# Kernel tuning notes

Hardware: AMD Instinct MI355X
Metric: run time of the kernel (lower is better)

The kernel has to match this reference:

```python
import jax, jax.numpy as jnp
import numpy as np
from jax import lax

C, H, W = 16, 1536, 1536
KS = 5    # shift kernel size
PS = 17   # patch size (odd -> conv with padding PS//2 returns exactly HxW)


def setup_inputs() -> dict:
    key = jax.random.key(0)
    ks = jax.random.split(key, 8)
    return {
        "key_vec": jax.random.normal(ks[0], (C,), jnp.float32),
        "beta": jax.random.normal(ks[1], (), jnp.float32),
        "gate": jax.random.normal(ks[2], (), jnp.float32),
        "shift": jax.random.normal(ks[3], (KS, KS), jnp.float32),
        "sharpen": jax.random.normal(ks[4], (), jnp.float32),
        "prev_weights": jax.random.uniform(ks[5], (H, W), jnp.float32),
        "patch": jax.random.normal(ks[6], (C, PS, PS), jnp.float32),
        "mem": jax.random.normal(ks[7], (C, H, W), jnp.float32),
    }


def _address(key_vec, beta, gate, shift, sharpen, prev_weights, mem):
    eps = 1e-8
    c, h, w = mem.shape
    flat_mem = mem.reshape(c, -1).T                       # [HW, C]
    key_norm = key_vec / jnp.maximum(jnp.linalg.norm(key_vec), eps)
    mem_norm = flat_mem / jnp.maximum(
        jnp.linalg.norm(flat_mem, axis=1, keepdims=True), eps)
    content_sim = mem_norm @ key_norm                      # [HW]
    beta_pos = jax.nn.softplus(beta)
    w_c = jax.nn.softmax(beta_pos * content_sim)
    g = jax.nn.sigmoid(gate)
    w_g = g * w_c + (1.0 - g) * prev_weights.reshape(-1)
    # circular-shift convolution (torch conv2d = cross-correlation)
    sk = jax.nn.softmax(shift.reshape(-1)).reshape(shift.shape)
    pad = sk.shape[0] // 2
    padded = jnp.pad(w_g.reshape(h, w), ((pad, pad), (pad, pad)), mode="wrap")
    shifted = lax.conv_general_dilated(
        padded[None, None], sk[None, None], (1, 1), "VALID",
        dimension_numbers=("NCHW", "OIHW", "NCHW"))[0, 0]   # [H, W]
    zeta = jax.nn.softplus(sharpen) + 1.0
    w_pow = jnp.clip(shifted, 1e-8, None) ** zeta
    return w_pow / jnp.maximum(w_pow.sum(), 1e-6)          # [H, W]


def _apply_weighted_patch(weights, patch):
    # torch: conv2d(weights, flipped patch, padding=center) == true convolution,
    # i.e. scatter-add of patch at every cell scaled by weights.
    s = patch.shape[-1]
    center = s // 2
    kernels = patch[:, ::-1, ::-1][:, None]                # [C, 1, S, S]
    out = lax.conv_general_dilated(
        weights[None, None], kernels, (1, 1),
        [(center, center), (center, center)],
        dimension_numbers=("NCHW", "OIHW", "NCHW"))[0]     # [C, H, W]
    return out


def reference(key_vec, beta, gate, shift, sharpen, prev_weights, patch, mem):
    w = _address(key_vec, beta, gate, shift, sharpen, prev_weights, mem)
    contrib = _apply_weighted_patch(w, patch)
    return mem + contrib
```

## Files before the change

kernel.cpp:

```cpp
#include <hip/hip_runtime.h>
#include <math.h>

#define HH 1536
#define WW 1536
#define HWN (HH*WW)
#define CC 16
#define KSZ 5
#define PS 17
#define ISTR 128
#define NMF 26
#define NQ 52

typedef __bf16 bf16x8 __attribute__((ext_vector_type(8)));
typedef float f32x16 __attribute__((ext_vector_type(16)));

union Frag { uint4 u4; bf16x8 b8; };

__device__ inline unsigned short f32_to_bf16(float v) {
  unsigned int b = __float_as_uint(v);
  unsigned int r = (b + 0x7FFFu + ((b >> 16) & 1u)) >> 16;
  return (unsigned short)r;
}

__device__ inline float softplusf(float x) {
  return x > 20.f ? x : log1pf(expf(x));
}

__device__ inline float waveSum(float v) {
#pragma unroll
  for (int o = 32; o; o >>= 1) v += __shfl_xor(v, o);
  return v;
}

__global__ void k_scoreexp(const float* __restrict__ mem, const float* __restrict__ key,
                           const float* __restrict__ beta, float* __restrict__ e,
                           float* __restrict__ red) {
  __shared__ float sm[4];
  float kv[CC];
  float kn = 0.f;
#pragma unroll
  for (int c = 0; c < CC; c++) { kv[c] = key[c]; kn += kv[c] * kv[c]; }
  float bp = softplusf(beta[0]);
  float scale = bp / fmaxf(sqrtf(kn), 1e-8f);

  int hw4 = (blockIdx.x * 256 + threadIdx.x) * 4;
  float d0 = 0.f, d1 = 0.f, d2 = 0.f, d3 = 0.f;
  float n0 = 0.f, n1 = 0.f, n2 = 0.f, n3 = 0.f;
#pragma unroll
  for (int c = 0; c < CC; c++) {
    float4 m = *reinterpret_cast<const float4*>(mem + (size_t)c * HWN + hw4);
    d0 += m.x * kv[c]; d1 += m.y * kv[c]; d2 += m.z * kv[c]; d3 += m.w * kv[c];
    n0 += m.x * m.x;   n1 += m.y * m.y;   n2 += m.z * m.z;   n3 += m.w * m.w;
  }
  float4 ev;
  ev.x = expf(scale * d0 / fmaxf(sqrtf(n0), 1e-8f) - bp);
  ev.y = expf(scale * d1 / fmaxf(sqrtf(n1), 1e-8f) - bp);
  ev.z = expf(scale * d2 / fmaxf(sqrtf(n2), 1e-8f) - bp);
  ev.w = expf(scale * d3 / fmaxf(sqrtf(n3), 1e-8f) - bp);
  *reinterpret_cast<float4*>(e + hw4) = ev;

  float lsum = waveSum(ev.x + ev.y + ev.z + ev.w);
  if ((threadIdx.x & 63) == 0) sm[threadIdx.x >> 6] = lsum;
  __syncthreads();
  if (threadIdx.x == 0) red[blockIdx.x] = sm[0] + sm[1] + sm[2] + sm[3];
}

__global__ void k_mid1(const float* __restrict__ red, float* __restrict__ scal,
                       const float* __restrict__ shift, float* __restrict__ skb,
                       const float* __restrict__ gate) {
  __shared__ float sm[256];
  float s = 0.f;
  for (int i = threadIdx.x; i < 2304; i += 256) s += red[i];
  sm[threadIdx.x] = s;
  __syncthreads();
  for (int st = 128; st; st >>= 1) {
    if (threadIdx.x < st) sm[threadIdx.x] += sm[threadIdx.x + st];
    __syncthreads();
  }
  if (threadIdx.x == 0) {
    float S = sm[0];
    float g = 1.f / (1.f + expf(-gate[0]));
    scal[3] = g / S;
    scal[4] = 1.f - g;
    float mx = -INFINITY;
    for (int i = 0; i < KSZ * KSZ; i++) mx = fmaxf(mx, shift[i]);
    float ee[KSZ * KSZ];
    float sum = 0.f;
    for (int i = 0; i < KSZ * KSZ; i++) { ee[i] = expf(shift[i] - mx); sum += ee[i]; }
    for (int i = 0; i < KSZ * KSZ; i++) skb[i] = ee[i] / sum;
  }
}

__global__ void k_shiftf(const float* __restrict__ e, const float* __restrict__ prev,
                         const float* __restrict__ scal, const float* __restrict__ skb,
                         const float* __restrict__ sharpen, unsigned short* __restrict__ tbf,
                         float* __restrict__ red) {
  __shared__ float tile[20][21];
  __shared__ float sks[KSZ * KSZ];
  __shared__ float sm[4];
  int tx = threadIdx.x & 15, ty = threadIdx.x >> 4;
  int x0 = blockIdx.x * 16, y0 = blockIdx.y * 16;
  if (threadIdx.x < KSZ * KSZ) sks[threadIdx.x] = skb[threadIdx.x];
  float gS = scal[3], og = scal[4];
  for (int i = threadIdx.x; i < 400; i += 256) {
    int r = i / 20, c = i % 20;
    int gy = (y0 + r - 2 + HH) % HH;
    int gx = (x0 + c - 2 + WW) % WW;
    int idx = gy * WW + gx;
    tile[r][c] = gS * e[idx] + og * prev[idx];
  }
  __syncthreads();
  float zeta = softplusf(sharpen[0]) + 1.f;
  float acc = 0.f;
#pragma unroll
  for (int i = 0; i < KSZ; i++)
#pragma unroll
    for (int j = 0; j < KSZ; j++)
      acc += sks[i * KSZ + j] * tile[ty + i][tx + j];
  float tp = powf(fmaxf(acc, 1e-8f), zeta);
  tbf[(y0 + ty) * WW + x0 + tx] = f32_to_bf16(tp);
  float lsum = waveSum(tp);
  if ((threadIdx.x & 63) == 0) sm[threadIdx.x >> 6] = lsum;
  __syncthreads();
  if (threadIdx.x == 0) red[blockIdx.y * 96 + blockIdx.x] = sm[0] + sm[1] + sm[2] + sm[3];
}

__global__ void k_mid2(const float* __restrict__ red, float* __restrict__ scal,
                       const float* __restrict__ patch, unsigned short* __restrict__ afrag) {
  __shared__ float sm[256];
  __shared__ float sInv;
  float s = 0.f;
  for (int i = threadIdx.x; i < 9216; i += 256) s += red[i];
  sm[threadIdx.x] = s;
  __syncthreads();
  for (int st = 128; st; st >>= 1) {
    if (threadIdx.x < st) sm[threadIdx.x] += sm[threadIdx.x + st];
    __syncthreads();
  }
  if (threadIdx.x == 0) { sInv = 1.f / fmaxf(sm[0], 1e-6f); scal[2] = sInv; }
  __syncthreads();
  float invS = sInv;
  for (int idx = threadIdx.x; idx < NQ * 32 * 8; idx += 256) {
    int j = idx & 7;
    int m = (idx >> 3) & 31;
    int q = idx >> 8;
    int c = m & 15, p = m >> 4;
    int k = q * 8 + j;
    int vv = k / 24;
    int u2 = k % 24;
    int u = 17 - u2 + p;
    float val = 0.f;
    if (vv <= 16 && u >= 0 && u <= 16) val = patch[(c * PS + u) * PS + vv] * invS;
    afrag[idx] = f32_to_bf16(val);
  }
}

__global__ void __launch_bounds__(512, 8) k_conv17w(
    const unsigned short* __restrict__ tbf, const unsigned short* __restrict__ afrag,
    const float* __restrict__ mem, float* __restrict__ out) {
  __shared__ __align__(16) unsigned short ca[48 * ISTR];
  int tid = threadIdx.x;
  int x0 = blockIdx.x * 32;
  int y00 = blockIdx.y * 64 + blockIdx.z * 2;
  int yBase = y00 - 9;

  for (int idx = tid; idx < 480; idx += 512) {
    int X = idx % 48, oct = idx / 48;
    int x = x0 - 8 + X;
    bool xok = (x >= 0) && (x < WW);
    int yb = yBase + oct * 8;
    unsigned short sv[8];
#pragma unroll
    for (int j = 0; j < 8; j++) {
      int y = yb + j;
      sv[j] = (xok && y >= 0 && y < HH) ? tbf[y * WW + x] : (unsigned short)0;
    }
    uint4 qv;
    qv.x = (unsigned)sv[0] | ((unsigned)sv[1] << 16);
    qv.y = (unsigned)sv[2] | ((unsigned)sv[3] << 16);
    qv.z = (unsigned)sv[4] | ((unsigned)sv[5] << 16);
    qv.w = (unsigned)sv[6] | ((unsigned)sv[7] << 16);
    int slot = (oct ^ (X & 7) ^ (X >> 3)) & 15;
    int boff = X * (ISTR * 2) + (slot << 4);
    *reinterpret_cast<uint4*>(reinterpret_cast<char*>(ca) + boff) = qv;
  }
  __syncthreads();

  int lane = tid & 63;
  int t = tid >> 6;
  int col = lane & 31, h1 = lane >> 5;

  f32x16 acc;
#pragma unroll
  for (int i = 0; i < 16; i++) acc[i] = 0.f;

  Frag Acur;
  Acur.u4 = *reinterpret_cast<const uint4*>(afrag + (h1 * 32 + col) * 8);
  int vv = 0, rr = h1;

#pragma unroll 1
  for (int e = 0; e < NMF; e++) {
    Frag Anext;
    if (e + 1 < NMF) {
      int qn = 2 * (e + 1) + h1;
      Anext.u4 = *reinterpret_cast<const uint4*>(afrag + (qn * 32 + col) * 8);
    }
    int X = col + 16 - vv;
    if (X < 0) X = 0;
    int xs = (X & 7) ^ (X >> 3);
    int oc = t + rr;
    int boff = X * (ISTR * 2) + (((oc ^ xs) & 15) << 4);
    Frag B;
    B.u4 = *reinterpret_cast<const uint4*>(reinterpret_cast<const char*>(ca) + boff);
    acc = __builtin_amdgcn_mfma_f32_32x32x16_bf16(Acur.b8, B.b8, acc, 0, 0, 0);
    if (e + 1 < NMF) Acur = Anext;
    rr += 2;
    if (rr >= 3) { rr -= 3; vv += 1; }
  }

  int xo = x0 + col;
  int b = y00 + 8 * t;
#pragma unroll
  for (int reg = 0; reg < 16; reg++) {
    int row = (reg & 3) + 8 * (reg >> 2) + 4 * h1;
    int c = row & 15;
    int p = row >> 4;
    size_t off = (size_t)c * HWN + (size_t)(b + p) * WW + xo;
    out[off] = mem[off] + acc[reg];
  }
}

extern "C" void kernel_launch(void* const* d_in, const int* in_sizes, int n_in,
                              void* d_out, int out_size, void* d_ws, size_t ws_size,
                              hipStream_t stream) {
  const float* key     = (const float*)d_in[0];
  const float* beta    = (const float*)d_in[1];
  const float* gate    = (const float*)d_in[2];
  const float* shift   = (const float*)d_in[3];
  const float* sharpen = (const float*)d_in[4];
  const float* prev    = (const float*)d_in[5];
  const float* patch   = (const float*)d_in[6];
  const float* mem     = (const float*)d_in[7];
  float* out = (float*)d_out;

  float* ws = (float*)d_ws;
  unsigned short* tbf = (unsigned short*)ws;
  float* red  = ws + HWN / 2;
  float* scal = red + 9216;
  float* skb  = scal + 16;
  unsigned short* afrag = (unsigned short*)(skb + 32);

  float* e = out;

  k_scoreexp<<<2304, 256, 0, stream>>>(mem, key, beta, e, red);
  k_mid1<<<1, 256, 0, stream>>>(red, scal, shift, skb, gate);
  dim3 g2(96, 96);
  k_shiftf<<<g2, 256, 0, stream>>>(e, prev, scal, skb, sharpen, tbf, red);
  k_mid2<<<1, 256, 0, stream>>>(red, scal, patch, afrag);
  dim3 g3(48, 24, 4);
  k_conv17w<<<g3, 512, 0, stream>>>(tbf, afrag, mem, out);
}
```

Baseline: 164.4 us.

## Fully unroll MFMA loop, add interior fast path for tile load, relax launch bounds

The 26-step MFMA loop is now fully unrolled with compile-time shift/slot indices, and A fragments are loaded directly from global memory instead of software-prefetched. The shared-memory tile load gets a branch-free interior path that skips per-element bounds checks, and the LDS swizzle drops the X>>3 term. The launch bound minimum occupancy drops from 8 to 6 to give the unrolled loop more registers. This trades some occupancy and a possibly different LDS bank-conflict pattern for less index arithmetic and more instruction-level parallelism.

Measured after the change: 162.4 us. Within noise of the previous version (-1.2%).

```diff
diff --git a/kernel.cpp b/kernel.cpp
--- a/kernel.cpp
+++ b/kernel.cpp
@@ -155,7 +155,7 @@
   }
 }
 
-__global__ void __launch_bounds__(512, 8) k_conv17w(
+__global__ void __launch_bounds__(512, 6) k_conv17w(
     const unsigned short* __restrict__ tbf, const unsigned short* __restrict__ afrag,
     const float* __restrict__ mem, float* __restrict__ out) {
   __shared__ __align__(16) unsigned short ca[48 * ISTR];
@@ -164,25 +164,42 @@
   int y00 = blockIdx.y * 64 + blockIdx.z * 2;
   int yBase = y00 - 9;
 
-  for (int idx = tid; idx < 480; idx += 512) {
-    int X = idx % 48, oct = idx / 48;
-    int x = x0 - 8 + X;
-    bool xok = (x >= 0) && (x < WW);
-    int yb = yBase + oct * 8;
-    unsigned short sv[8];
-#pragma unroll
-    for (int j = 0; j < 8; j++) {
-      int y = yb + j;
-      sv[j] = (xok && y >= 0 && y < HH) ? tbf[y * WW + x] : (unsigned short)0;
+  bool interior = (x0 >= 8) && (x0 + 40 <= WW) && (yBase >= 0) && (yBase + 80 <= HH);
+  if (interior) {
+    for (int idx = tid; idx < 480; idx += 512) {
+      int X = idx % 48, oct = idx / 48;
+      const unsigned short* p = tbf + (size_t)(yBase + oct * 8) * WW + (x0 - 8 + X);
+      unsigned short sv[8];
+#pragma unroll
+      for (int j = 0; j < 8; j++) sv[j] = p[(size_t)j * WW];
+      uint4 qv;
+      qv.x = (unsigned)sv[0] | ((unsigned)sv[1] << 16);
+      qv.y = (unsigned)sv[2] | ((unsigned)sv[3] << 16);
+      qv.z = (unsigned)sv[4] | ((unsigned)sv[5] << 16);
+      qv.w = (unsigned)sv[6] | ((unsigned)sv[7] << 16);
+      int slot = (oct ^ (X & 7)) & 15;
+      *reinterpret_cast<uint4*>(reinterpret_cast<char*>(ca) + X * (ISTR * 2) + (slot << 4)) = qv;
     }
-    uint4 qv;
-    qv.x = (unsigned)sv[0] | ((unsigned)sv[1] << 16);
-    qv.y = (unsigned)sv[2] | ((unsigned)sv[3] << 16);
-    qv.z = (unsigned)sv[4] | ((unsigned)sv[5] << 16);
-    qv.w = (unsigned)sv[6] | ((unsigned)sv[7] << 16);
-    int slot = (oct ^ (X & 7) ^ (X >> 3)) & 15;
-    int boff = X * (ISTR * 2) + (slot << 4);
-    *reinterpret_cast<uint4*>(reinterpret_cast<char*>(ca) + boff) = qv;
+  } else {
+    for (int idx = tid; idx < 480; idx += 512) {
+      int X = idx % 48, oct = idx / 48;
+      int x = x0 - 8 + X;
+      bool xok = (x >= 0) && (x < WW);
+      int yb = yBase + oct * 8;
+      unsigned short sv[8];
+#pragma unroll
+      for (int j = 0; j < 8; j++) {
+        int y = yb + j;
+        sv[j] = (xok && y >= 0 && y < HH) ? tbf[(size_t)y * WW + x] : (unsigned short)0;
+      }
+      uint4 qv;
+      qv.x = (unsigned)sv[0] | ((unsigned)sv[1] << 16);
+      qv.y = (unsigned)sv[2] | ((unsigned)sv[3] << 16);
+      qv.z = (unsigned)sv[4] | ((unsigned)sv[5] << 16);
+      qv.w = (unsigned)sv[6] | ((unsigned)sv[7] << 16);
+      int slot = (oct ^ (X & 7)) & 15;
+      *reinterpret_cast<uint4*>(reinterpret_cast<char*>(ca) + X * (ISTR * 2) + (slot << 4)) = qv;
+    }
   }
   __syncthreads();
 
@@ -194,28 +211,24 @@
 #pragma unroll
   for (int i = 0; i < 16; i++) acc[i] = 0.f;
 
-  Frag Acur;
-  Acur.u4 = *reinterpret_cast<const uint4*>(afrag + (h1 * 32 + col) * 8);
-  int vv = 0, rr = h1;
-
-#pragma unroll 1
+  const unsigned short* pa = afrag + ((size_t)h1 * 32 + col) * 8;
+  const char* cab = reinterpret_cast<const char*>(ca);
+
+#pragma unroll
   for (int e = 0; e < NMF; e++) {
-    Frag Anext;
-    if (e + 1 < NMF) {
-      int qn = 2 * (e + 1) + h1;
-      Anext.u4 = *reinterpret_cast<const uint4*>(afrag + (qn * 32 + col) * 8);
-    }
+    const int q0 = 2 * e;
+    const int vv0 = q0 / 3,       rr0 = q0 % 3;
+    const int vv1 = (q0 + 1) / 3, rr1 = (q0 + 1) % 3;
+    int vv = h1 ? vv1 : vv0;
+    int rr = h1 ? rr1 : rr0;
     int X = col + 16 - vv;
     if (X < 0) X = 0;
-    int xs = (X & 7) ^ (X >> 3);
-    int oc = t + rr;
-    int boff = X * (ISTR * 2) + (((oc ^ xs) & 15) << 4);
+    int slot = ((t + rr) ^ (X & 7)) & 15;
     Frag B;
-    B.u4 = *reinterpret_cast<const uint4*>(reinterpret_cast<const char*>(ca) + boff);
-    acc = __builtin_amdgcn_mfma_f32_32x32x16_bf16(Acur.b8, B.b8, acc, 0, 0, 0);
-    if (e + 1 < NMF) Acur = Anext;
-    rr += 2;
-    if (rr >= 3) { rr -= 3; vv += 1; }
+    B.u4 = *reinterpret_cast<const uint4*>(cab + X * (ISTR * 2) + (slot << 4));
+    Frag A;
+    A.u4 = *reinterpret_cast<const uint4*>(pa + (size_t)e * 512);
+    acc = __builtin_amdgcn_mfma_f32_32x32x16_bf16(A.b8, B.b8, acc, 0, 0, 0);
   }
 
   int xo = x0 + col;
```
